# Optimization experiments

Hardware: AMD Instinct MI355X
Metric: run time of the kernel (lower is better)

The kernel has to match this reference:

```python
import jax, jax.numpy as jnp
import numpy as np


def setup_inputs() -> dict:
    key = jax.random.key(0)
    k1, k2 = jax.random.split(key)
    n_nodes, n_feat, n_edges = 100000, 64, 1600000
    x = jax.random.normal(k1, (n_nodes, n_feat), dtype=jnp.float32)
    edge_index = jax.random.randint(k2, (2, n_edges), 0, n_nodes, dtype=jnp.int64)
    return {"x": x, "edge_index": edge_index}


def reference(x, edge_index):
    # Faithful JAX version of OneHopGCNNormNodeLabelAggregator.forward:
    #   adj = SparseTensor.from_edge_index(edge_index)  (values = 1)
    #   adj_norm = gcn_norm(adj)  -> add self-loops (diag=1), symmetric D^-1/2 A D^-1/2
    #   x_neighbors = adj_norm.t() @ x
    n = x.shape[0]
    self_loops = jnp.arange(n, dtype=edge_index.dtype)
    row = jnp.concatenate([edge_index[0], self_loops])  # source of adj entry A[row, col]
    col = jnp.concatenate([edge_index[1], self_loops])
    # degree over rows (sparsesum dim=1 after fill_diag)
    deg = jax.ops.segment_sum(jnp.ones(row.shape, x.dtype), row, num_segments=n)
    deg_inv_sqrt = jnp.where(deg > 0, jax.lax.rsqrt(deg), 0.0).astype(x.dtype)
    # symmetric norm weight per edge
    w = deg_inv_sqrt[row] * deg_inv_sqrt[col]  # [E+n]
    # adj_norm.t() @ x : out[col] += w * x[row]
    x_neighbors = jax.ops.segment_sum(w[:, None] * x[row], col, num_segments=n)
    return x_neighbors
```

## Files before the change

### kernel.cpp

```cpp
#include <hip/hip_runtime.h>

#define NFEAT 64
#define BSHIFT 8
#define BCOLS 256
#define NBMAX 512
#define CAP 5120
#define CHUNK 3136
#define PT 512
#define NITP 7
#define FT 512
#define UT 512
#define FBIT (CAP / UT)
#define QCAP 1664


__device__ __forceinline__ unsigned short f2bf(float f) {
    unsigned int u = __float_as_uint(f);
    return (unsigned short)((u + 0x7FFFu + ((u >> 16) & 1u)) >> 16);
}

__device__ __forceinline__ float bflo(unsigned int u) {
    return __uint_as_float(u << 16);
}
__device__ __forceinline__ float bfhi(unsigned int u) {
    return __uint_as_float(u & 0xFFFF0000u);
}

__device__ __forceinline__ int wave_incl_scan(int v, int lane) {
    #pragma unroll
    for (int off = 1; off < 64; off <<= 1) {
        int u = __shfl_up(v, off);
        if (lane >= off) v += u;
    }
    return v;
}

__global__ void k_init(int* __restrict__ bcur, int* __restrict__ bcurR) {
    int t = threadIdx.x;
    bcur[t]  = t * CAP;
    bcurR[t] = t * CAP;
}

__global__ __launch_bounds__(PT)
void k_partCR(const int* __restrict__ rows, const int* __restrict__ cols,
              int* __restrict__ bcur, int* __restrict__ bcurR,
              int* __restrict__ part, unsigned char* __restrict__ partR, int E) {
    __shared__ int histC[NBMAX];
    __shared__ int histR[NBMAX];
    __shared__ int gbaseC[NBMAX];
    __shared__ int gbaseR[NBMAX];
    __shared__ int wsumC[8];
    __shared__ int wsumR[8];
    __shared__ int stageC[CHUNK];
    __shared__ unsigned char stageR[CHUNK];
    __shared__ unsigned short bidC[CHUNK];
    __shared__ unsigned short bidR[CHUNK];
    int chunk0 = blockIdx.x * CHUNK;
    int cnt = min(CHUNK, E - chunk0);
    int t = threadIdx.x;
    int lane = t & 63, wid = t >> 6;

    histC[t] = 0; histR[t] = 0;
    __syncthreads();

    int pk[NITP];
    unsigned char rpk[NITP];
    unsigned short cb[NITP], rb[NITP];
    #pragma unroll
    for (int k = 0; k < NITP; k++) {
        int i = t + k * PT;
        if (i < cnt) {
            int c = cols[chunk0 + i];
            int r = rows[chunk0 + i];
            int b  = c >> BSHIFT;
            int b2 = r >> BSHIFT;
            pk[k]  = ((c & (BCOLS - 1)) << 17) | r;
            rpk[k] = (unsigned char)(r & (BCOLS - 1));
            cb[k] = (unsigned short)b;
            rb[k] = (unsigned short)b2;
            atomicAdd(&histC[b], 1);
            atomicAdd(&histR[b2], 1);
        }
    }
    __syncthreads();

    int v1 = histC[t];
    int inc1 = wave_incl_scan(v1, lane);
    if (lane == 63) wsumC[wid] = inc1;
    int v2 = histR[t];
    int inc2 = wave_incl_scan(v2, lane);
    if (lane == 63) wsumR[wid] = inc2;
    __syncthreads();
    int addC = 0, addR = 0;
    #pragma unroll
    for (int k = 0; k < 8; k++) {
        if (k < wid) { addC += wsumC[k]; addR += wsumR[k]; }
    }
    int exC = inc1 - v1 + addC;
    int exR = inc2 - v2 + addR;
    gbaseC[t] = (v1 > 0) ? (atomicAdd(&bcur[t], v1) - exC) : 0;
    gbaseR[t] = (v2 > 0) ? (atomicAdd(&bcurR[t], v2) - exR) : 0;
    histC[t] = exC;
    histR[t] = exR;
    __syncthreads();

    #pragma unroll
    for (int k = 0; k < NITP; k++) {
        int i = t + k * PT;
        if (i < cnt) {
            int p = atomicAdd(&histC[cb[k]], 1);
            stageC[p] = pk[k];
            bidC[p] = cb[k];
            int p2 = atomicAdd(&histR[rb[k]], 1);
            stageR[p2] = rpk[k];
            bidR[p2] = rb[k];
        }
    }
    __syncthreads();
    for (int p = t; p < cnt; p += PT) {
        int b = bidC[p];
        int idx = gbaseC[b] + p;
        if (idx < (b + 1) * CAP) part[idx] = stageC[p];
        int b2 = bidR[p];
        int idx2 = gbaseR[b2] + p;
        if (idx2 < (b2 + 1) * CAP) partR[idx2] = stageR[p];
    }
}

__global__ __launch_bounds__(FT)
void k_fillR(const unsigned char* __restrict__ partR, const int* __restrict__ bcurR,
             const float4* __restrict__ x4, float* __restrict__ dinv,
             ushort4* __restrict__ xs4, int n) {
    __shared__ int lcnt[128];
    __shared__ float ldinv[128];
    int bh = blockIdx.x;
    int b = bh >> 1, half = bh & 1;
    int s = b * CAP;
    int t = threadIdx.x;

    int cntR = min(bcurR[b] - s, CAP);
    if (t < 128) lcnt[t] = 0;
    __syncthreads();
    for (int i = t; i < cntR; i += FT) {
        int key = partR[s + i];
        if ((key >> 7) == half) atomicAdd(&lcnt[key & 127], 1);
    }
    __syncthreads();
    int rows_base = (b << BSHIFT) + (half << 7);
    if (t < 128) {
        float d = rsqrtf((float)(lcnt[t] + 1));
        ldinv[t] = d;
        int gr = rows_base + t;
        if (gr < n) dinv[gr] = d;
    }
    __syncthreads();
    size_t base4 = (size_t)rows_base << 4;
    int nr = n - rows_base;
    if (nr <= 0) return;
    int lim = min(128, nr) << 4;
    for (int i = t; i < lim; i += FT) {
        float dd = ldinv[i >> 4];
        float4 vv = x4[base4 + i];
        ushort4 o;
        o.x = f2bf(dd * vv.x); o.y = f2bf(dd * vv.y);
        o.z = f2bf(dd * vv.z); o.w = f2bf(dd * vv.w);
        xs4[base4 + i] = o;
    }
}

__global__ __launch_bounds__(UT)
void k_fuse(const int* __restrict__ part, const int* __restrict__ bcur,
            const unsigned short* __restrict__ xs,
            const float* __restrict__ dinv,
            float4* __restrict__ out4, int n) {
    __shared__ int lcnt[64];
    __shared__ int lps[64];
    __shared__ int cur[64];
    __shared__ int stage[QCAP];
    int qb = blockIdx.x;
    int b = qb >> 2, q = qb & 3;
    int s = b * CAP;
    int cnt = min(bcur[b] - s, CAP);
    int t = threadIdx.x;

    if (t < 64) lcnt[t] = 0;
    __syncthreads();

    int pk[FBIT];
    #pragma unroll
    for (int k = 0; k < FBIT; k++) {
        int i = t + k * UT;
        int v2 = (i < cnt) ? part[s + i] : -1;
        pk[k] = v2;
        if (v2 >= 0) {
            int c = v2 >> 17;
            if ((c >> 6) == q) atomicAdd(&lcnt[c & 63], 1);
        }
    }
    __syncthreads();

    if (t < 64) {
        int v = lcnt[t];
        int inc = wave_incl_scan(v, t);
        int ex = inc - v;
        lps[t] = ex;
        cur[t] = ex;
    }
    __syncthreads();

    #pragma unroll
    for (int k = 0; k < FBIT; k++) {
        int v2 = pk[k];
        if (v2 >= 0) {
            int c = v2 >> 17;
            if ((c >> 6) == q) {
                int p = atomicAdd(&cur[c & 63], 1);
                if (p < QCAP) stage[p] = v2 & 0x1FFFF;
            }
        }
    }
    __syncthreads();

    int g = t >> 3, li = t & 7;
    int node = (b << BSHIFT) + (q << 6) + g;
    if (node >= n) return;
    int ss = lps[g];
    int len = lcnt[g];
    if (ss + len > QCAP) len = QCAP > ss ? QCAP - ss : 0;
    float a0 = 0.f, a1 = 0.f, a2 = 0.f, a3 = 0.f;
    float a4 = 0.f, a5 = 0.f, a6 = 0.f, a7 = 0.f;
    int npair = len >> 1;
    uint4 u0, u1;
    if (npair > 0) {
        int r0 = stage[ss], r1 = stage[ss + 1];
        u0 = *((const uint4*)(xs + ((size_t)r0 << 6)) + li);
        u1 = *((const uint4*)(xs + ((size_t)r1 << 6)) + li);
    }
    for (int qq = 1; qq < npair; qq++) {
        int p = ss + qq * 2;
        int r0 = stage[p], r1 = stage[p + 1];
        uint4 n0 = *((const uint4*)(xs + ((size_t)r0 << 6)) + li);
        uint4 n1 = *((const uint4*)(xs + ((size_t)r1 << 6)) + li);
        a0 += bflo(u0.x); a1 += bfhi(u0.x);
        a2 += bflo(u0.y); a3 += bfhi(u0.y);
        a4 += bflo(u0.z); a5 += bfhi(u0.z);
        a6 += bflo(u0.w); a7 += bfhi(u0.w);
        a0 += bflo(u1.x); a1 += bfhi(u1.x);
        a2 += bflo(u1.y); a3 += bfhi(u1.y);
        a4 += bflo(u1.z); a5 += bfhi(u1.z);
        a6 += bflo(u1.w); a7 += bfhi(u1.w);
        u0 = n0; u1 = n1;
    }
    if (npair > 0) {
        a0 += bflo(u0.x); a1 += bfhi(u0.x);
        a2 += bflo(u0.y); a3 += bfhi(u0.y);
        a4 += bflo(u0.z); a5 += bfhi(u0.z);
        a6 += bflo(u0.w); a7 += bfhi(u0.w);
        a0 += bflo(u1.x); a1 += bfhi(u1.x);
        a2 += bflo(u1.y); a3 += bfhi(u1.y);
        a4 += bflo(u1.z); a5 += bfhi(u1.z);
        a6 += bflo(u1.w); a7 += bfhi(u1.w);
    }
    if (len & 1) {
        int r = stage[ss + len - 1];
        uint4 u = *((const uint4*)(xs + ((size_t)r << 6)) + li);
        a0 += bflo(u.x); a1 += bfhi(u.x);
        a2 += bflo(u.y); a3 += bfhi(u.y);
        a4 += bflo(u.z); a5 += bfhi(u.z);
        a6 += bflo(u.w); a7 += bfhi(u.w);
    }
    float dc = dinv[node];
    uint4 us = *((const uint4*)(xs + ((size_t)node << 6)) + li);
    float4 r0o, r1o;
    r0o.x = dc * (a0 + bflo(us.x));
    r0o.y = dc * (a1 + bfhi(us.x));
    r0o.z = dc * (a2 + bflo(us.y));
    r0o.w = dc * (a3 + bfhi(us.y));
    r1o.x = dc * (a4 + bflo(us.z));
    r1o.y = dc * (a5 + bfhi(us.z));
    r1o.z = dc * (a6 + bflo(us.w));
    r1o.w = dc * (a7 + bfhi(us.w));
    size_t ob = ((size_t)node << 4) + (li << 1);
    out4[ob] = r0o;
    out4[ob + 1] = r1o;
}

extern "C" void kernel_launch(void* const* d_in, const int* in_sizes, int n_in,
                              void* d_out, int out_size, void* d_ws, size_t ws_size,
                              hipStream_t stream) {
    const float* x    = (const float*)d_in[0];
    const int*   eidx = (const int*)d_in[1];

    const int n = in_sizes[0] / NFEAT;
    const int E = in_sizes[1] / 2;
    const int* rows = eidx;
    const int* cols = eidx + E;
    float* out = (float*)d_out;

    const int nbuck = (n + BCOLS - 1) >> BSHIFT;

    char* w = (char*)d_ws;
    int*   bcur  = (int*)w;     w += NBMAX * 4;
    int*   bcurR = (int*)w;     w += NBMAX * 4;
    float* dinv  = (float*)w;   w += (size_t)n * 4;
    w = (char*)(((uintptr_t)w + 15) & ~(uintptr_t)15);
    unsigned short* xs = (unsigned short*)w;  w += (size_t)n * NFEAT * 2;
    int*   part  = (int*)w;     w += (size_t)nbuck * CAP * 4;
    unsigned char* partR = (unsigned char*)w;

    k_init<<<1, NBMAX, 0, stream>>>(bcur, bcurR);

    int nchunk = (E + CHUNK - 1) / CHUNK;
    k_partCR<<<nchunk, PT, 0, stream>>>(rows, cols, bcur, bcurR, part, partR, E);
    k_fillR<<<nbuck * 2, FT, 0, stream>>>(partR, bcurR, (const float4*)x,
                                          dinv, (ushort4*)xs, n);
    k_fuse<<<nbuck * 4, UT, 0, stream>>>(part, bcur, xs, dinv,
                                         (float4*)out, n);
}
```

Baseline: 143.1 us.

## Fuse partition, fill and aggregate phases into one cooperative persistent kernel

Merges the init, partition, row-degree/fill and aggregation kernels into a single cooperative kernel that uses grid-wide syncs between phases and loops blocks over the work items. Bucket counters are zeroed with a memset and become relative offsets. The fill phase now works on 64-row quarters instead of 128-row halves. This removes several kernel launch gaps and tail drains. In exchange it caps the grid at 512 resident blocks, adds grid barriers, and keeps the separate-kernel path as a fallback.

```diff
diff --git a/kernel.cpp b/kernel.cpp
--- a/kernel.cpp
+++ b/kernel.cpp
@@ -1,4 +1,7 @@
 #include <hip/hip_runtime.h>
+#include <hip/hip_cooperative_groups.h>
+
+namespace cg = cooperative_groups;
 
 #define NFEAT 64
 #define BSHIFT 8
@@ -6,19 +9,30 @@
 #define NBMAX 512
 #define CAP 5120
 #define CHUNK 3136
-#define PT 512
 #define NITP 7
-#define FT 512
-#define UT 512
-#define FBIT (CAP / UT)
+#define TPB 512
+#define FBIT (CAP / TPB)
 #define QCAP 1664
-
+#define GRIDMAX 512
+
+
+struct SmemPart {
+    int histC[NBMAX]; int histR[NBMAX];
+    int gbaseC[NBMAX]; int gbaseR[NBMAX];
+    int wsumC[8]; int wsumR[8];
+    int stageC[CHUNK];
+    unsigned short bidC[CHUNK];
+    unsigned short bidR[CHUNK];
+    unsigned char stageR[CHUNK];
+};
+struct SmemFill { int lcnt[64]; float ldinv[64]; };
+struct SmemFuse { int lcnt[64]; int lps[64]; int cur[64]; int stage[QCAP]; };
+union SmemAll { SmemPart p; SmemFill f; SmemFuse u; };
 
 __device__ __forceinline__ unsigned short f2bf(float f) {
     unsigned int u = __float_as_uint(f);
     return (unsigned short)((u + 0x7FFFu + ((u >> 16) & 1u)) >> 16);
 }
-
 __device__ __forceinline__ float bflo(unsigned int u) {
     return __uint_as_float(u << 16);
 }
@@ -35,32 +49,18 @@
     return v;
 }
 
-__global__ void k_init(int* __restrict__ bcur, int* __restrict__ bcurR) {
-    int t = threadIdx.x;
-    bcur[t]  = t * CAP;
-    bcurR[t] = t * CAP;
-}
-
-__global__ __launch_bounds__(PT)
-void k_partCR(const int* __restrict__ rows, const int* __restrict__ cols,
-              int* __restrict__ bcur, int* __restrict__ bcurR,
-              int* __restrict__ part, unsigned char* __restrict__ partR, int E) {
-    __shared__ int histC[NBMAX];
-    __shared__ int histR[NBMAX];
-    __shared__ int gbaseC[NBMAX];
-    __shared__ int gbaseR[NBMAX];
-    __shared__ int wsumC[8];
-    __shared__ int wsumR[8];
-    __shared__ int stageC[CHUNK];
-    __shared__ unsigned char stageR[CHUNK];
-    __shared__ unsigned short bidC[CHUNK];
-    __shared__ unsigned short bidR[CHUNK];
-    int chunk0 = blockIdx.x * CHUNK;
-    int cnt = min(CHUNK, E - chunk0);
+
+__device__ __forceinline__ void phase_part(
+        SmemPart& sp, int ch,
+        const int* __restrict__ rows, const int* __restrict__ cols,
+        int* __restrict__ bcur, int* __restrict__ bcurR,
+        int* __restrict__ part, unsigned char* __restrict__ partR, int E) {
     int t = threadIdx.x;
     int lane = t & 63, wid = t >> 6;
-
-    histC[t] = 0; histR[t] = 0;
+    int chunk0 = ch * CHUNK;
+    int cnt = min(CHUNK, E - chunk0);
+
+    sp.histC[t] = 0; sp.histR[t] = 0;
     __syncthreads();
 
     int pk[NITP];
@@ -68,7 +68,7 @@
     unsigned short cb[NITP], rb[NITP];
     #pragma unroll
     for (int k = 0; k < NITP; k++) {
-        int i = t + k * PT;
+        int i = t + k * TPB;
         if (i < cnt) {
             int c = cols[chunk0 + i];
             int r = rows[chunk0 + i];
@@ -78,133 +78,128 @@
             rpk[k] = (unsigned char)(r & (BCOLS - 1));
             cb[k] = (unsigned short)b;
             rb[k] = (unsigned short)b2;
-            atomicAdd(&histC[b], 1);
-            atomicAdd(&histR[b2], 1);
-        }
-    }
-    __syncthreads();
-
-    int v1 = histC[t];
+            atomicAdd(&sp.histC[b], 1);
+            atomicAdd(&sp.histR[b2], 1);
+        }
+    }
+    __syncthreads();
+
+    int v1 = sp.histC[t];
     int inc1 = wave_incl_scan(v1, lane);
-    if (lane == 63) wsumC[wid] = inc1;
-    int v2 = histR[t];
+    if (lane == 63) sp.wsumC[wid] = inc1;
+    int v2 = sp.histR[t];
     int inc2 = wave_incl_scan(v2, lane);
-    if (lane == 63) wsumR[wid] = inc2;
+    if (lane == 63) sp.wsumR[wid] = inc2;
     __syncthreads();
     int addC = 0, addR = 0;
     #pragma unroll
     for (int k = 0; k < 8; k++) {
-        if (k < wid) { addC += wsumC[k]; addR += wsumR[k]; }
+        if (k < wid) { addC += sp.wsumC[k]; addR += sp.wsumR[k]; }
     }
     int exC = inc1 - v1 + addC;
     int exR = inc2 - v2 + addR;
-    gbaseC[t] = (v1 > 0) ? (atomicAdd(&bcur[t], v1) - exC) : 0;
-    gbaseR[t] = (v2 > 0) ? (atomicAdd(&bcurR[t], v2) - exR) : 0;
-    histC[t] = exC;
-    histR[t] = exR;
+    sp.gbaseC[t] = (v1 > 0) ? (t * CAP + atomicAdd(&bcur[t],  v1) - exC) : 0;
+    sp.gbaseR[t] = (v2 > 0) ? (t * CAP + atomicAdd(&bcurR[t], v2) - exR) : 0;
+    sp.histC[t] = exC;
+    sp.histR[t] = exR;
     __syncthreads();
 
     #pragma unroll
     for (int k = 0; k < NITP; k++) {
-        int i = t + k * PT;
+        int i = t + k * TPB;
         if (i < cnt) {
-            int p = atomicAdd(&histC[cb[k]], 1);
-            stageC[p] = pk[k];
-            bidC[p] = cb[k];
-            int p2 = atomicAdd(&histR[rb[k]], 1);
-            stageR[p2] = rpk[k];
-            bidR[p2] = rb[k];
-        }
-    }
-    __syncthreads();
-    for (int p = t; p < cnt; p += PT) {
-        int b = bidC[p];
-        int idx = gbaseC[b] + p;
-        if (idx < (b + 1) * CAP) part[idx] = stageC[p];
-        int b2 = bidR[p];
-        int idx2 = gbaseR[b2] + p;
-        if (idx2 < (b2 + 1) * CAP) partR[idx2] = stageR[p];
-    }
-}
-
-__global__ __launch_bounds__(FT)
-void k_fillR(const unsigned char* __restrict__ partR, const int* __restrict__ bcurR,
-             const float4* __restrict__ x4, float* __restrict__ dinv,
-             ushort4* __restrict__ xs4, int n) {
-    __shared__ int lcnt[128];
-    __shared__ float ldinv[128];
-    int bh = blockIdx.x;
-    int b = bh >> 1, half = bh & 1;
+            int p = atomicAdd(&sp.histC[cb[k]], 1);
+            sp.stageC[p] = pk[k];
+            sp.bidC[p] = cb[k];
+            int p2 = atomicAdd(&sp.histR[rb[k]], 1);
+            sp.stageR[p2] = rpk[k];
+            sp.bidR[p2] = rb[k];
+        }
+    }
+    __syncthreads();
+    for (int p = t; p < cnt; p += TPB) {
+        int b = sp.bidC[p];
+        int idx = sp.gbaseC[b] + p;
+        if (idx < (b + 1) * CAP) part[idx] = sp.stageC[p];
+        int b2 = sp.bidR[p];
+        int idx2 = sp.gbaseR[b2] + p;
+        if (idx2 < (b2 + 1) * CAP) partR[idx2] = sp.stageR[p];
+    }
+    __syncthreads();
+}
+
+__device__ __forceinline__ void phase_fill(
+        SmemFill& sf, int qb,
+        const unsigned char* __restrict__ partR, const int* __restrict__ bcurR,
+        const float4* __restrict__ x4, float* __restrict__ dinv,
+        unsigned short* __restrict__ xs, int n) {
+    int t = threadIdx.x;
+    int b = qb >> 2, q = qb & 3;
     int s = b * CAP;
-    int t = threadIdx.x;
-
-    int cntR = min(bcurR[b] - s, CAP);
-    if (t < 128) lcnt[t] = 0;
-    __syncthreads();
-    for (int i = t; i < cntR; i += FT) {
+    int cntR = min(bcurR[b], CAP);
+    if (t < 64) sf.lcnt[t] = 0;
+    __syncthreads();
+    for (int i = t; i < cntR; i += TPB) {
         int key = partR[s + i];
-        if ((key >> 7) == half) atomicAdd(&lcnt[key & 127], 1);
-    }
-    __syncthreads();
-    int rows_base = (b << BSHIFT) + (half << 7);
-    if (t < 128) {
-        float d = rsqrtf((float)(lcnt[t] + 1));
-        ldinv[t] = d;
+        if ((key >> 6) == q) atomicAdd(&sf.lcnt[key & 63], 1);
+    }
+    __syncthreads();
+    int rows_base = (b << BSHIFT) + (q << 6);
+    if (t < 64) {
+        float d = rsqrtf((float)(sf.lcnt[t] + 1));
+        sf.ldinv[t] = d;
         int gr = rows_base + t;
         if (gr < n) dinv[gr] = d;
     }
     __syncthreads();
-    size_t base4 = (size_t)rows_base << 4;
     int nr = n - rows_base;
-    if (nr <= 0) return;
-    int lim = min(128, nr) << 4;
-    for (int i = t; i < lim; i += FT) {
-        float dd = ldinv[i >> 4];
-        float4 vv = x4[base4 + i];
-        ushort4 o;
-        o.x = f2bf(dd * vv.x); o.y = f2bf(dd * vv.y);
-        o.z = f2bf(dd * vv.z); o.w = f2bf(dd * vv.w);
-        xs4[base4 + i] = o;
-    }
-}
-
-__global__ __launch_bounds__(UT)
-void k_fuse(const int* __restrict__ part, const int* __restrict__ bcur,
-            const unsigned short* __restrict__ xs,
-            const float* __restrict__ dinv,
-            float4* __restrict__ out4, int n) {
-    __shared__ int lcnt[64];
-    __shared__ int lps[64];
-    __shared__ int cur[64];
-    __shared__ int stage[QCAP];
-    int qb = blockIdx.x;
+    if (nr > 0) {
+        size_t base4 = (size_t)rows_base << 4;
+        int lim = min(64, nr) << 4;
+        for (int i = t; i < lim; i += TPB) {
+            float dd = sf.ldinv[i >> 4];
+            float4 vv = x4[base4 + i];
+            ushort4 o;
+            o.x = f2bf(dd * vv.x); o.y = f2bf(dd * vv.y);
+            o.z = f2bf(dd * vv.z); o.w = f2bf(dd * vv.w);
+            ((ushort4*)xs)[base4 + i] = o;
+        }
+    }
+    __syncthreads();
+}
+
+__device__ __forceinline__ void phase_fuse(
+        SmemFuse& su, int qb,
+        const int* __restrict__ part, const int* __restrict__ bcur,
+        const unsigned short* __restrict__ xs, const float* __restrict__ dinv,
+        float4* __restrict__ out4, int n) {
+    int t = threadIdx.x;
     int b = qb >> 2, q = qb & 3;
     int s = b * CAP;
-    int cnt = min(bcur[b] - s, CAP);
-    int t = threadIdx.x;
-
-    if (t < 64) lcnt[t] = 0;
+    int cnt = min(bcur[b], CAP);
+
+    if (t < 64) su.lcnt[t] = 0;
     __syncthreads();
 
     int pk[FBIT];
     #pragma unroll
     for (int k = 0; k < FBIT; k++) {
-        int i = t + k * UT;
+        int i = t + k * TPB;
         int v2 = (i < cnt) ? part[s + i] : -1;
         pk[k] = v2;
         if (v2 >= 0) {
             int c = v2 >> 17;
-            if ((c >> 6) == q) atomicAdd(&lcnt[c & 63], 1);
+            if ((c >> 6) == q) atomicAdd(&su.lcnt[c & 63], 1);
         }
     }
     __syncthreads();
 
     if (t < 64) {
-        int v = lcnt[t];
+        int v = su.lcnt[t];
         int inc = wave_incl_scan(v, t);
         int ex = inc - v;
-        lps[t] = ex;
-        cur[t] = ex;
+        su.lps[t] = ex;
+        su.cur[t] = ex;
     }
     __syncthreads();
 
@@ -214,8 +209,8 @@
         if (v2 >= 0) {
             int c = v2 >> 17;
             if ((c >> 6) == q) {
-                int p = atomicAdd(&cur[c & 63], 1);
-                if (p < QCAP) stage[p] = v2 & 0x1FFFF;
+                int p = atomicAdd(&su.cur[c & 63], 1);
+                if (p < QCAP) su.stage[p] = v2 & 0x1FFFF;
             }
         }
     }
@@ -223,66 +218,119 @@
 
     int g = t >> 3, li = t & 7;
     int node = (b << BSHIFT) + (q << 6) + g;
-    if (node >= n) return;
-    int ss = lps[g];
-    int len = lcnt[g];
-    if (ss + len > QCAP) len = QCAP > ss ? QCAP - ss : 0;
-    float a0 = 0.f, a1 = 0.f, a2 = 0.f, a3 = 0.f;
-    float a4 = 0.f, a5 = 0.f, a6 = 0.f, a7 = 0.f;
-    int npair = len >> 1;
-    uint4 u0, u1;
-    if (npair > 0) {
-        int r0 = stage[ss], r1 = stage[ss + 1];
-        u0 = *((const uint4*)(xs + ((size_t)r0 << 6)) + li);
-        u1 = *((const uint4*)(xs + ((size_t)r1 << 6)) + li);
-    }
-    for (int qq = 1; qq < npair; qq++) {
-        int p = ss + qq * 2;
-        int r0 = stage[p], r1 = stage[p + 1];
-        uint4 n0 = *((const uint4*)(xs + ((size_t)r0 << 6)) + li);
-        uint4 n1 = *((const uint4*)(xs + ((size_t)r1 << 6)) + li);
-        a0 += bflo(u0.x); a1 += bfhi(u0.x);
-        a2 += bflo(u0.y); a3 += bfhi(u0.y);
-        a4 += bflo(u0.z); a5 += bfhi(u0.z);
-        a6 += bflo(u0.w); a7 += bfhi(u0.w);
-        a0 += bflo(u1.x); a1 += bfhi(u1.x);
-        a2 += bflo(u1.y); a3 += bfhi(u1.y);
-        a4 += bflo(u1.z); a5 += bfhi(u1.z);
-        a6 += bflo(u1.w); a7 += bfhi(u1.w);
-        u0 = n0; u1 = n1;
-    }
-    if (npair > 0) {
-        a0 += bflo(u0.x); a1 += bfhi(u0.x);
-        a2 += bflo(u0.y); a3 += bfhi(u0.y);
-        a4 += bflo(u0.z); a5 += bfhi(u0.z);
-        a6 += bflo(u0.w); a7 += bfhi(u0.w);
-        a0 += bflo(u1.x); a1 += bfhi(u1.x);
-        a2 += bflo(u1.y); a3 += bfhi(u1.y);
-        a4 += bflo(u1.z); a5 += bfhi(u1.z);
-        a6 += bflo(u1.w); a7 += bfhi(u1.w);
-    }
-    if (len & 1) {
-        int r = stage[ss + len - 1];
-        uint4 u = *((const uint4*)(xs + ((size_t)r << 6)) + li);
-        a0 += bflo(u.x); a1 += bfhi(u.x);
-        a2 += bflo(u.y); a3 += bfhi(u.y);
-        a4 += bflo(u.z); a5 += bfhi(u.z);
-        a6 += bflo(u.w); a7 += bfhi(u.w);
-    }
-    float dc = dinv[node];
-    uint4 us = *((const uint4*)(xs + ((size_t)node << 6)) + li);
-    float4 r0o, r1o;
-    r0o.x = dc * (a0 + bflo(us.x));
-    r0o.y = dc * (a1 + bfhi(us.x));
-    r0o.z = dc * (a2 + bflo(us.y));
-    r0o.w = dc * (a3 + bfhi(us.y));
-    r1o.x = dc * (a4 + bflo(us.z));
-    r1o.y = dc * (a5 + bfhi(us.z));
-    r1o.z = dc * (a6 + bflo(us.w));
-    r1o.w = dc * (a7 + bfhi(us.w));
-    size_t ob = ((size_t)node << 4) + (li << 1);
-    out4[ob] = r0o;
-    out4[ob + 1] = r1o;
+    if (node < n) {
+        int ss = su.lps[g];
+        int len = su.lcnt[g];
+        if (ss + len > QCAP) len = QCAP > ss ? QCAP - ss : 0;
+        float a0 = 0.f, a1 = 0.f, a2 = 0.f, a3 = 0.f;
+        float a4 = 0.f, a5 = 0.f, a6 = 0.f, a7 = 0.f;
+        int npair = len >> 1;
+        uint4 u0, u1;
+        if (npair > 0) {
+            int r0 = su.stage[ss], r1 = su.stage[ss + 1];
+            u0 = *((const uint4*)(xs + ((size_t)r0 << 6)) + li);
+            u1 = *((const uint4*)(xs + ((size_t)r1 << 6)) + li);
+        }
+        for (int qq = 1; qq < npair; qq++) {
+            int p = ss + qq * 2;
+            int r0 = su.stage[p], r1 = su.stage[p + 1];
+            uint4 n0 = *((const uint4*)(xs + ((size_t)r0 << 6)) + li);
+            uint4 n1 = *((const uint4*)(xs + ((size_t)r1 << 6)) + li);
+            a0 += bflo(u0.x); a1 += bfhi(u0.x);
+            a2 += bflo(u0.y); a3 += bfhi(u0.y);
+            a4 += bflo(u0.z); a5 += bfhi(u0.z);
+            a6 += bflo(u0.w); a7 += bfhi(u0.w);
+            a0 += bflo(u1.x); a1 += bfhi(u1.x);
+            a2 += bflo(u1.y); a3 += bfhi(u1.y);
+            a4 += bflo(u1.z); a5 += bfhi(u1.z);
+            a6 += bflo(u1.w); a7 += bfhi(u1.w);
+            u0 = n0; u1 = n1;
+        }
+        if (npair > 0) {
+            a0 += bflo(u0.x); a1 += bfhi(u0.x);
+            a2 += bflo(u0.y); a3 += bfhi(u0.y);
+            a4 += bflo(u0.z); a5 += bfhi(u0.z);
+            a6 += bflo(u0.w); a7 += bfhi(u0.w);
+            a0 += bflo(u1.x); a1 += bfhi(u1.x);
+            a2 += bflo(u1.y); a3 += bfhi(u1.y);
+            a4 += bflo(u1.z); a5 += bfhi(u1.z);
+            a6 += bflo(u1.w); a7 += bfhi(u1.w);
+        }
+        if (len & 1) {
+            int r = su.stage[ss + len - 1];
+            uint4 u = *((const uint4*)(xs + ((size_t)r << 6)) + li);
+            a0 += bflo(u.x); a1 += bfhi(u.x);
+            a2 += bflo(u.y); a3 += bfhi(u.y);
+            a4 += bflo(u.z); a5 += bfhi(u.z);
+            a6 += bflo(u.w); a7 += bfhi(u.w);
+        }
+        float dc = dinv[node];
+        uint4 us = *((const uint4*)(xs + ((size_t)node << 6)) + li);
+        float4 r0o, r1o;
+        r0o.x = dc * (a0 + bflo(us.x));
+        r0o.y = dc * (a1 + bfhi(us.x));
+        r0o.z = dc * (a2 + bflo(us.y));
+        r0o.w = dc * (a3 + bfhi(us.y));
+        r1o.x = dc * (a4 + bflo(us.z));
+        r1o.y = dc * (a5 + bfhi(us.z));
+        r1o.z = dc * (a6 + bflo(us.w));
+        r1o.w = dc * (a7 + bfhi(us.w));
+        size_t ob = ((size_t)node << 4) + (li << 1);
+        out4[ob] = r0o;
+        out4[ob + 1] = r1o;
+    }
+    __syncthreads();
+}
+
+
+__global__ __launch_bounds__(TPB, 4)
+void k_all(const int* __restrict__ rows, const int* __restrict__ cols,
+           const float4* __restrict__ x4,
+           int* __restrict__ bcur, int* __restrict__ bcurR,
+           int* __restrict__ part, unsigned char* __restrict__ partR,
+           float* __restrict__ dinv, unsigned short* __restrict__ xs,
+           float4* __restrict__ out4, int n, int E, int nbuck) {
+    __shared__ SmemAll sm;
+    cg::grid_group grid = cg::this_grid();
+
+    int nchunk = (E + CHUNK - 1) / CHUNK;
+    for (int ch = blockIdx.x; ch < nchunk; ch += gridDim.x)
+        phase_part(sm.p, ch, rows, cols, bcur, bcurR, part, partR, E);
+    grid.sync();
+
+    int nq = nbuck * 4;
+    for (int qb = blockIdx.x; qb < nq; qb += gridDim.x)
+        phase_fill(sm.f, qb, partR, bcurR, x4, dinv, xs, n);
+    grid.sync();
+
+    for (int qb = blockIdx.x; qb < nq; qb += gridDim.x)
+        phase_fuse(sm.u, qb, part, bcur, xs, dinv, out4, n);
+}
+
+
+__global__ __launch_bounds__(TPB)
+void k_partCR(const int* __restrict__ rows, const int* __restrict__ cols,
+              int* __restrict__ bcur, int* __restrict__ bcurR,
+              int* __restrict__ part, unsigned char* __restrict__ partR, int E) {
+    __shared__ SmemPart sp;
+    phase_part(sp, blockIdx.x, rows, cols, bcur, bcurR, part, partR, E);
+}
+
+__global__ __launch_bounds__(TPB)
+void k_fillR(const unsigned char* __restrict__ partR, const int* __restrict__ bcurR,
+             const float4* __restrict__ x4, float* __restrict__ dinv,
+             unsigned short* __restrict__ xs, int n) {
+    __shared__ SmemFill sf;
+    phase_fill(sf, blockIdx.x, partR, bcurR, x4, dinv, xs, n);
+}
+
+__global__ __launch_bounds__(TPB)
+void k_fuse(const int* __restrict__ part, const int* __restrict__ bcur,
+            const unsigned short* __restrict__ xs,
+            const float* __restrict__ dinv,
+            float4* __restrict__ out4, int n) {
+    __shared__ SmemFuse su;
+    phase_fuse(su, blockIdx.x, part, bcur, xs, dinv, out4, n);
 }
 
 extern "C" void kernel_launch(void* const* d_in, const int* in_sizes, int n_in,
@@ -291,13 +339,12 @@
     const float* x    = (const float*)d_in[0];
     const int*   eidx = (const int*)d_in[1];
 
-    const int n = in_sizes[0] / NFEAT;
-    const int E = in_sizes[1] / 2;
+    int n = in_sizes[0] / NFEAT;
+    int E = in_sizes[1] / 2;
     const int* rows = eidx;
     const int* cols = eidx + E;
-    float* out = (float*)d_out;
-
-    const int nbuck = (n + BCOLS - 1) >> BSHIFT;
+
+    int nbuck = (n + BCOLS - 1) >> BSHIFT;
 
     char* w = (char*)d_ws;
     int*   bcur  = (int*)w;     w += NBMAX * 4;
@@ -308,12 +355,39 @@
     int*   part  = (int*)w;     w += (size_t)nbuck * CAP * 4;
     unsigned char* partR = (unsigned char*)w;
 
-    k_init<<<1, NBMAX, 0, stream>>>(bcur, bcurR);
-
-    int nchunk = (E + CHUNK - 1) / CHUNK;
-    k_partCR<<<nchunk, PT, 0, stream>>>(rows, cols, bcur, bcurR, part, partR, E);
-    k_fillR<<<nbuck * 2, FT, 0, stream>>>(partR, bcurR, (const float4*)x,
-                                          dinv, (ushort4*)xs, n);
-    k_fuse<<<nbuck * 4, UT, 0, stream>>>(part, bcur, xs, dinv,
-                                         (float4*)out, n);
-}
+    const float4* x4 = (const float4*)x;
+    float4* out4 = (float4*)d_out;
+
+    hipMemsetAsync(bcur, 0, NBMAX * 2 * 4, stream);
+
+    static int coopGrid = -1;
+    if (coopGrid < 0) {
+        int bpc = 0, ncu = 0, dev = 0;
+        hipGetDevice(&dev);
+        hipDeviceGetAttribute(&ncu, hipDeviceAttributeMultiprocessorCount, dev);
+        hipOccupancyMaxActiveBlocksPerMultiprocessor(&bpc, (const void*)k_all,
+                                                     TPB, 0);
+        coopGrid = (bpc > 0 && ncu > 0) ? min(GRIDMAX, bpc * ncu) : 0;
+    }
+
+    bool done = false;
+    if (coopGrid > 0) {
+        void* args[] = {(void*)&rows, (void*)&cols, (void*)&x4,
+                        (void*)&bcur, (void*)&bcurR,
+                        (void*)&part, (void*)&partR,
+                        (void*)&dinv, (void*)&xs, (void*)&out4,
+                        (void*)&n, (void*)&E, (void*)&nbuck};
+        hipError_t err = hipLaunchCooperativeKernel((const void*)k_all,
+                                                    dim3(coopGrid), dim3(TPB),
+                                                    args, 0, stream);
+        done = (err == hipSuccess);
+        if (!done) coopGrid = 0;
+    }
+    if (!done) {
+        int nchunk = (E + CHUNK - 1) / CHUNK;
+        k_partCR<<<nchunk, TPB, 0, stream>>>(rows, cols, bcur, bcurR,
+                                             part, partR, E);
+        k_fillR<<<nbuck * 4, TPB, 0, stream>>>(partR, bcurR, x4, dinv, xs, n);
+        k_fuse<<<nbuck * 4, TPB, 0, stream>>>(part, bcur, xs, dinv, out4, n);
+    }
+}
```

New measurement: 267.5 us. 1.87x slower.
